# Optimization experiments

Measured on AMD Instinct MI355X. Metric: run time of the kernel, lower is better.

## Reference

```python
import jax, jax.numpy as jnp
import numpy as np

K = 20      # self.k in OurModel
TAU = 1.0   # self.tau in OurModel


def _knn_feats(emb, idx, yctx):
    # emb: [N, E] embedding table; idx: [B] int query ids; yctx: [B, N] residual context
    a = emb[idx]                                            # [B, E] gathered query embeddings
    # squared euclidean via gram trick, then sqrt == torch.cdist(p=2)
    d2 = (jnp.sum(a * a, axis=-1, keepdims=True)
          + jnp.sum(emb * emb, axis=-1)[None, :]
          - 2.0 * a @ emb.T)                                 # [B, N]
    sim = jnp.sqrt(jnp.clip(d2, 0.0, None)) + 0.001
    rows = jnp.arange(idx.shape[0])
    sim = sim.at[rows, idx].set(0.0)                         # zero self-distance
    w = jnp.exp(-sim / TAU)                                  # [B, N], self weight == 1 (max)
    # top (K+1) weights; drop the largest (the self entry) -> top-K neighbours.
    # Matches torch argsort(w)[:, -(K+1):-1]; downstream ops are order-invariant reductions.
    topw, topi = jax.lax.top_k(w, K + 1)
    topw = topw[:, 1:]                                       # [B, K]
    sel = jnp.take_along_axis(yctx, topi[:, 1:], axis=1)     # [B, K]
    f1 = jnp.sum(topw, axis=1)                               # sum of weights
    f2 = jnp.sum(sel * topw, axis=1) / jnp.sum(topw, axis=1) # weighted mean
    f3 = jnp.std(sel, axis=1, ddof=1)                        # torch.std is unbiased
    return f1, f2, f3


def _forward(emb0, emb1, rctx0, rctx1, idx0, idx1, mean_in, std_in,
             W1, b1, Wm, bm, Ws, bs):
    a1, a2, a3 = _knn_feats(emb0, idx0, rctx0)
    b1_, b2_, b3_ = _knn_feats(emb1, idx1, rctx1)
    # torch.cat(final1 + final2 + final3 + [mean, std]) column order
    feats = jnp.stack([a1, b1_, a2, b2_, a3, b3_, mean_in, std_in], axis=1)  # [B, 8]
    h = jnp.maximum(feats @ W1 + b1, 0.0)                    # [B, 64]
    mean_out = h @ Wm + bm[0]                                # [B]
    std_out = h @ Ws + bs[0]                                 # [B]
    return mean_out, std_out


def setup_inputs() -> dict:
    key = jax.random.key(0)
    ks = jax.random.split(key, 14)
    B, N, E, H = 512, 50000, 16, 64
    return {
        "emb0": jax.random.normal(ks[0], (N, E), jnp.float32),
        "emb1": jax.random.normal(ks[1], (N, E), jnp.float32),
        "rctx0": jax.random.normal(ks[2], (B, N), jnp.float32),
        "rctx1": jax.random.normal(ks[3], (B, N), jnp.float32),
        "idx0": jax.random.randint(ks[4], (B,), 0, N, jnp.int32),
        "idx1": jax.random.randint(ks[5], (B,), 0, N, jnp.int32),
        "mean_in": jax.random.normal(ks[6], (B,), jnp.float32),
        "std_in": jax.random.normal(ks[7], (B,), jnp.float32),
        "W1": jax.random.normal(ks[8], (8, H), jnp.float32) * 0.1,
        "b1": jax.random.normal(ks[9], (H,), jnp.float32) * 0.1,
        "Wm": jax.random.normal(ks[10], (H,), jnp.float32) * 0.1,
        "bm": jax.random.normal(ks[11], (1,), jnp.float32) * 0.1,
        "Ws": jax.random.normal(ks[12], (H,), jnp.float32) * 0.1,
        "bs": jax.random.normal(ks[13], (1,), jnp.float32) * 0.1,
    }


def reference(emb0, emb1, rctx0, rctx1, idx0, idx1, mean_in, std_in,
              W1, b1, Wm, bm, Ws, bs):
    return _forward(emb0, emb1, rctx0, rctx1, idx0, idx1, mean_in, std_in,
                    W1, b1, Wm, bm, Ws, bs)
```

## Files before the change

kernel.cpp:

```cpp
#include <hip/hip_runtime.h>
#include <math.h>

typedef unsigned long long u64;
#define INF64 0xFFFFFFFFFFFFFFFFULL
#define FBIG 3.3e38f
#define NTA 256
#define KSEL 20
#define QB 4
#define CNK 8
#define PREF 4
#define CAP 384

static __device__ __forceinline__ u64 umin64(u64 a, u64 b) { return a < b ? a : b; }

static __device__ __forceinline__ float dot16(
    float4 a0, float4 a1, float4 a2, float4 a3,
    float4 b0, float4 b1, float4 b2, float4 b3)
{
    float d = 0.f;
    d = fmaf(a0.x, b0.x, d); d = fmaf(a0.y, b0.y, d);
    d = fmaf(a0.z, b0.z, d); d = fmaf(a0.w, b0.w, d);
    d = fmaf(a1.x, b1.x, d); d = fmaf(a1.y, b1.y, d);
    d = fmaf(a1.z, b1.z, d); d = fmaf(a1.w, b1.w, d);
    d = fmaf(a2.x, b2.x, d); d = fmaf(a2.y, b2.y, d);
    d = fmaf(a2.z, b2.z, d); d = fmaf(a2.w, b2.w, d);
    d = fmaf(a3.x, b3.x, d); d = fmaf(a3.y, b3.y, d);
    d = fmaf(a3.z, b3.z, d); d = fmaf(a3.w, b3.w, d);
    return d;
}

__global__ __launch_bounds__(NTA) void knn_scan_kernel(
    const float* __restrict__ emb0, const float* __restrict__ emb1,
    const int* __restrict__ idx0, const int* __restrict__ idx1,
    u64* __restrict__ chunkTop, int N, int B)
{
    const int tid = threadIdx.x;
    const int lane = tid & 63;
    const int wv = tid >> 6;
    const int bx = blockIdx.x;
    const int xcd = bx & 7;
    const int s = xcd & 1;
    const int t = (bx >> 3) * 4 + (xcd >> 1);
    const int c = t & (CNK - 1);
    const int g = t >> 3;

    const float* __restrict__ emb = s ? emb1 : emb0;
    const int* __restrict__ idxp = s ? idx1 : idx0;
    const int qbase = QB * g;
    const int self0 = idxp[qbase + 0];
    const int self1 = idxp[qbase + 1];
    const int self2 = idxp[qbase + 2];
    const int self3 = idxp[qbase + 3];

    const int chunkLen = (N + CNK - 1) / CNK;
    const int jbeg = c * chunkLen;
    const int jend = min(N, jbeg + chunkLen);

    float4 q00, q01, q02, q03, q10, q11, q12, q13;
    float4 q20, q21, q22, q23, q30, q31, q32, q33;
    { const float4* p = (const float4*)(emb + (size_t)self0 * 16); q00 = p[0]; q01 = p[1]; q02 = p[2]; q03 = p[3]; }
    { const float4* p = (const float4*)(emb + (size_t)self1 * 16); q10 = p[0]; q11 = p[1]; q12 = p[2]; q13 = p[3]; }
    { const float4* p = (const float4*)(emb + (size_t)self2 * 16); q20 = p[0]; q21 = p[1]; q22 = p[2]; q23 = p[3]; }
    { const float4* p = (const float4*)(emb + (size_t)self3 * 16); q30 = p[0]; q31 = p[1]; q32 = p[2]; q33 = p[3]; }
    const float na0 = dot16(q00, q01, q02, q03, q00, q01, q02, q03);
    const float na1 = dot16(q10, q11, q12, q13, q10, q11, q12, q13);
    const float na2 = dot16(q20, q21, q22, q23, q20, q21, q22, q23);
    const float na3 = dot16(q30, q31, q32, q33, q30, q31, q32, q33);

    __shared__ float sminf[QB][NTA];
    __shared__ u64 sbuf[QB][CAP];
    __shared__ int scnt[QB];
    __shared__ float sboundf[QB];

    float mn0 = FBIG, mn1 = FBIG, mn2 = FBIG, mn3 = FBIG;
#pragma unroll
    for (int k = 0; k < PREF; ++k) {
        const int j = jbeg + (k << 8) + tid;
        const float4* p = (const float4*)(emb + (size_t)j * 16);
        float4 e0 = p[0], e1 = p[1], e2 = p[2], e3 = p[3];
        const float ne = dot16(e0, e1, e2, e3, e0, e1, e2, e3);
        float dd;
        dd = fmaxf(fmaf(dot16(q00, q01, q02, q03, e0, e1, e2, e3), -2.f, na0 + ne), 0.f); mn0 = fminf(mn0, dd);
        dd = fmaxf(fmaf(dot16(q10, q11, q12, q13, e0, e1, e2, e3), -2.f, na1 + ne), 0.f); mn1 = fminf(mn1, dd);
        dd = fmaxf(fmaf(dot16(q20, q21, q22, q23, e0, e1, e2, e3), -2.f, na2 + ne), 0.f); mn2 = fminf(mn2, dd);
        dd = fmaxf(fmaf(dot16(q30, q31, q32, q33, e0, e1, e2, e3), -2.f, na3 + ne), 0.f); mn3 = fminf(mn3, dd);
    }
    sminf[0][tid] = mn0; sminf[1][tid] = mn1; sminf[2][tid] = mn2; sminf[3][tid] = mn3;
    if (tid < QB) scnt[tid] = 0;
    __syncthreads();

    {
        float v0 = sminf[wv][lane];
        float v1 = sminf[wv][lane + 64];
        float v2 = sminf[wv][lane + 128];
        float v3 = sminf[wv][lane + 192];
        float gm = 0.f;
        for (int r = 0; r < KSEL + 1; ++r) {
            float cm = fminf(fminf(v0, v1), fminf(v2, v3));
#pragma unroll
            for (int o = 32; o; o >>= 1) cm = fminf(cm, __shfl_xor(cm, o, 64));
            gm = cm;
            if (v0 == gm) v0 = FBIG;
            if (v1 == gm) v1 = FBIG;
            if (v2 == gm) v2 = FBIG;
            if (v3 == gm) v3 = FBIG;
        }
        if (lane == 0) sboundf[wv] = __uint_as_float(__float_as_uint(gm) + 2);
    }
    __syncthreads();
    const float bnd0 = sboundf[0], bnd1 = sboundf[1];
    const float bnd2 = sboundf[2], bnd3 = sboundf[3];

    for (int j = jbeg + tid; j < jend; j += NTA) {
        const float4* p = (const float4*)(emb + (size_t)j * 16);
        float4 e0 = p[0], e1 = p[1], e2 = p[2], e3 = p[3];
        const float ne = dot16(e0, e1, e2, e3, e0, e1, e2, e3);
        const float dd0 = fmaxf(fmaf(dot16(q00, q01, q02, q03, e0, e1, e2, e3), -2.f, na0 + ne), 0.f);
        const float dd1 = fmaxf(fmaf(dot16(q10, q11, q12, q13, e0, e1, e2, e3), -2.f, na1 + ne), 0.f);
        const float dd2 = fmaxf(fmaf(dot16(q20, q21, q22, q23, e0, e1, e2, e3), -2.f, na2 + ne), 0.f);
        const float dd3 = fmaxf(fmaf(dot16(q30, q31, q32, q33, e0, e1, e2, e3), -2.f, na3 + ne), 0.f);
        if (dd0 <= bnd0 && j != self0) {
            int sl = atomicAdd(&scnt[0], 1);
            if (sl < CAP) sbuf[0][sl] = ((u64)__float_as_uint(dd0) << 32) | (unsigned)j;
        }
        if (dd1 <= bnd1 && j != self1) {
            int sl = atomicAdd(&scnt[1], 1);
            if (sl < CAP) sbuf[1][sl] = ((u64)__float_as_uint(dd1) << 32) | (unsigned)j;
        }
        if (dd2 <= bnd2 && j != self2) {
            int sl = atomicAdd(&scnt[2], 1);
            if (sl < CAP) sbuf[2][sl] = ((u64)__float_as_uint(dd2) << 32) | (unsigned)j;
        }
        if (dd3 <= bnd3 && j != self3) {
            int sl = atomicAdd(&scnt[3], 1);
            if (sl < CAP) sbuf[3][sl] = ((u64)__float_as_uint(dd3) << 32) | (unsigned)j;
        }
    }
    __syncthreads();

    {
        const int M = min(scnt[wv], CAP);
        u64 t0 = (lane < M)       ? sbuf[wv][lane]       : INF64;
        u64 t1 = (lane + 64 < M)  ? sbuf[wv][lane + 64]  : INF64;
        u64 t2 = (lane + 128 < M) ? sbuf[wv][lane + 128] : INF64;
        u64 t3 = (lane + 192 < M) ? sbuf[wv][lane + 192] : INF64;
        u64 t4 = (lane + 256 < M) ? sbuf[wv][lane + 256] : INF64;
        u64 t5 = (lane + 320 < M) ? sbuf[wv][lane + 320] : INF64;
        u64 keep = INF64;
        for (int r = 0; r < KSEL; ++r) {
            u64 cm = umin64(umin64(umin64(t0, t1), umin64(t2, t3)), umin64(t4, t5));
#pragma unroll
            for (int o = 32; o; o >>= 1) cm = umin64(cm, __shfl_xor(cm, o, 64));
            if (t0 == cm) t0 = INF64;
            if (t1 == cm) t1 = INF64;
            if (t2 == cm) t2 = INF64;
            if (t3 == cm) t3 = INF64;
            if (t4 == cm) t4 = INF64;
            if (t5 == cm) t5 = INF64;
            if (lane == r) keep = cm;
        }
        if (lane < KSEL)
            chunkTop[(((size_t)(s * B + qbase + wv)) * CNK + c) * KSEL + lane] = keep;
    }
}

__global__ __launch_bounds__(128) void merge_mlp_kernel(
    const u64* __restrict__ chunkTop,
    const float* __restrict__ rctx0, const float* __restrict__ rctx1,
    const float* __restrict__ mean_in, const float* __restrict__ std_in,
    const float* __restrict__ W1, const float* __restrict__ b1,
    const float* __restrict__ Wm, const float* __restrict__ bm,
    const float* __restrict__ Ws, const float* __restrict__ bs,
    float* __restrict__ out, int N, int B)
{
    const int b = blockIdx.x;
    const int tid = threadIdx.x;
    const int s = tid >> 6;
    const int lane = tid & 63;
    __shared__ float sf[8];

    const u64* src = chunkTop + ((size_t)(s * B + b)) * CNK * KSEL;
    u64 v0 = src[lane];
    u64 v1 = src[lane + 64];
    u64 v2 = (lane < CNK * KSEL - 128) ? src[lane + 128] : INF64;
    u64 keep = INF64;
    for (int r = 0; r < KSEL; ++r) {
        u64 cm = umin64(v0, umin64(v1, v2));
#pragma unroll
        for (int o = 32; o; o >>= 1) cm = umin64(cm, __shfl_xor(cm, o, 64));
        if (v0 == cm) v0 = INF64;
        if (v1 == cm) v1 = INF64;
        if (v2 == cm) v2 = INF64;
        if (lane == r) keep = cm;
    }
    float w = 0.f, sv = 0.f;
    if (lane < KSEL) {
        float d2 = __uint_as_float((unsigned int)(keep >> 32));
        int j = (int)(unsigned int)(keep & 0xFFFFFFFFULL);
        float sim = sqrtf(d2) + 0.001f;
        w = expf(-sim);
        const float* __restrict__ rctx = s ? rctx1 : rctx0;
        sv = rctx[(size_t)b * N + j];
    }
    float sw = w, ssw = sv * w, ss = sv, ss2 = sv * sv;
#pragma unroll
    for (int o = 32; o; o >>= 1) {
        sw  += __shfl_down(sw,  o, 64);
        ssw += __shfl_down(ssw, o, 64);
        ss  += __shfl_down(ss,  o, 64);
        ss2 += __shfl_down(ss2, o, 64);
    }
    if (lane == 0) {
        sf[0 + s] = sw;
        sf[2 + s] = ssw / sw;
        float mean = ss * (1.f / KSEL);
        float var = (ss2 - (float)KSEL * mean * mean) * (1.f / (KSEL - 1));
        sf[4 + s] = sqrtf(fmaxf(var, 0.f));
        if (s == 0) { sf[6] = mean_in[b]; sf[7] = std_in[b]; }
    }
    __syncthreads();

    if (tid < 64) {
        float f0 = sf[0], f1 = sf[1], f2 = sf[2], f3 = sf[3];
        float f4 = sf[4], f5 = sf[5], f6 = sf[6], f7 = sf[7];
        float h = b1[lane];
        h = fmaf(f0, W1[0 * 64 + lane], h);
        h = fmaf(f1, W1[1 * 64 + lane], h);
        h = fmaf(f2, W1[2 * 64 + lane], h);
        h = fmaf(f3, W1[3 * 64 + lane], h);
        h = fmaf(f4, W1[4 * 64 + lane], h);
        h = fmaf(f5, W1[5 * 64 + lane], h);
        h = fmaf(f6, W1[6 * 64 + lane], h);
        h = fmaf(f7, W1[7 * 64 + lane], h);
        h = fmaxf(h, 0.f);
        float mo = h * Wm[lane], so = h * Ws[lane];
#pragma unroll
        for (int o = 32; o; o >>= 1) {
            mo += __shfl_down(mo, o, 64);
            so += __shfl_down(so, o, 64);
        }
        if (lane == 0) {
            out[b] = mo + bm[0];
            out[B + b] = so + bs[0];
        }
    }
}

extern "C" void kernel_launch(void* const* d_in, const int* in_sizes, int n_in,
                              void* d_out, int out_size, void* d_ws, size_t ws_size,
                              hipStream_t stream) {
    const float* emb0    = (const float*)d_in[0];
    const float* emb1    = (const float*)d_in[1];
    const float* rctx0   = (const float*)d_in[2];
    const float* rctx1   = (const float*)d_in[3];
    const int*   idx0    = (const int*)d_in[4];
    const int*   idx1    = (const int*)d_in[5];
    const float* mean_in = (const float*)d_in[6];
    const float* std_in  = (const float*)d_in[7];
    const float* W1      = (const float*)d_in[8];
    const float* b1      = (const float*)d_in[9];
    const float* Wm      = (const float*)d_in[10];
    const float* bm      = (const float*)d_in[11];
    const float* Ws      = (const float*)d_in[12];
    const float* bs      = (const float*)d_in[13];

    const int B = in_sizes[4];
    const int N = in_sizes[0] / 16;

    u64* chunkTop = (u64*)d_ws;

    knn_scan_kernel<<<dim3(2 * (B / QB) * CNK), NTA, 0, stream>>>(
        emb0, emb1, idx0, idx1, chunkTop, N, B);

    merge_mlp_kernel<<<dim3(B), 128, 0, stream>>>(
        chunkTop, rctx0, rctx1, mean_in, std_in,
        W1, b1, Wm, bm, Ws, bs, (float*)d_out, N, B);
}
```

Measured before the change: 301.7 us.

## Compute KNN distances with split-bf16 MFMA tiles and exact candidate rescoring

Replaces the per-thread scalar FP32 distance loop with 32x32x16 bf16 MFMA tiles. Each embedding is split into hi/lo bf16 parts so three MFMAs approximate the fp32 dot product. A separate kernel precomputes the embedding norms, and each block now handles 32 queries and 16 chunks, so embedding reuse across queries goes up. Candidates within a slack (DEPS=0.5) of the approximate threshold are rescored exactly in fp32 before top-k selection. The risks are approximation error versus the slack margin and overflow of the smaller candidate capacity, which is now 256.

```diff
diff --git a/kernel.cpp b/kernel.cpp
--- a/kernel.cpp
+++ b/kernel.cpp
@@ -2,16 +2,33 @@
 #include <math.h>
 
 typedef unsigned long long u64;
+typedef unsigned int u32;
 #define INF64 0xFFFFFFFFFFFFFFFFULL
 #define FBIG 3.3e38f
-#define NTA 256
 #define KSEL 20
-#define QB 4
-#define CNK 8
-#define PREF 4
-#define CAP 384
+#define QT   32
+#define CNK  16
+#define CAP  256
+#define PREFT 4
+#define DEPS 0.5f
+#define NTHR 512
+
+typedef __bf16 bf16x8 __attribute__((ext_vector_type(8)));
+typedef float  f32x16 __attribute__((ext_vector_type(16)));
+typedef unsigned int uint4e __attribute__((ext_vector_type(4)));
 
 static __device__ __forceinline__ u64 umin64(u64 a, u64 b) { return a < b ? a : b; }
+static __device__ __forceinline__ u32 asu(float f) { return __builtin_bit_cast(u32, f); }
+static __device__ __forceinline__ float trunchi(u32 u) { return __builtin_bit_cast(float, u & 0xffff0000u); }
+#define PERM2(a,b) __builtin_amdgcn_perm((a),(b),0x07060302u)
+static __device__ __forceinline__ bf16x8 mk8(u32 a, u32 b, u32 c, u32 d) {
+    uint4e t = {a, b, c, d};
+    return __builtin_bit_cast(bf16x8, t);
+}
+static __device__ __forceinline__ f32x16 zero16() {
+    f32x16 z = {0.f,0.f,0.f,0.f,0.f,0.f,0.f,0.f,0.f,0.f,0.f,0.f,0.f,0.f,0.f,0.f};
+    return z;
+}
 
 static __device__ __forceinline__ float dot16(
     float4 a0, float4 a1, float4 a2, float4 a3,
@@ -29,138 +46,212 @@
     return d;
 }
 
-__global__ __launch_bounds__(NTA) void knn_scan_kernel(
+static __device__ __forceinline__ void cvt_hilo(float4 f0, float4 f1, bf16x8& hi, bf16x8& lo) {
+    u32 u0=asu(f0.x),u1=asu(f0.y),u2=asu(f0.z),u3=asu(f0.w);
+    u32 u4=asu(f1.x),u5=asu(f1.y),u6=asu(f1.z),u7=asu(f1.w);
+    hi = mk8(PERM2(u1,u0), PERM2(u3,u2), PERM2(u5,u4), PERM2(u7,u6));
+    u32 w0=asu(f0.x-trunchi(u0)), w1=asu(f0.y-trunchi(u1));
+    u32 w2=asu(f0.z-trunchi(u2)), w3=asu(f0.w-trunchi(u3));
+    u32 w4=asu(f1.x-trunchi(u4)), w5=asu(f1.y-trunchi(u5));
+    u32 w6=asu(f1.z-trunchi(u6)), w7=asu(f1.w-trunchi(u7));
+    lo = mk8(PERM2(w1,w0), PERM2(w3,w2), PERM2(w5,w4), PERM2(w7,w6));
+}
+
+static __device__ __forceinline__ f32x16 tile_qe(
+    const float* __restrict__ embS, int base, int col, int kb, int N,
+    bf16x8 B1, bf16x8 B2)
+{
+    int row = base + col;
+    row = min(row, N - 1);
+    const float4* ep = (const float4*)(embS + (size_t)row * 16 + kb * 8);
+    float4 f0 = ep[0], f1 = ep[1];
+    bf16x8 A1, A2;
+    cvt_hilo(f0, f1, A1, A2);
+    f32x16 acc = zero16();
+    acc = __builtin_amdgcn_mfma_f32_32x32x16_bf16(A1, B1, acc, 0, 0, 0);
+    acc = __builtin_amdgcn_mfma_f32_32x32x16_bf16(A1, B2, acc, 0, 0, 0);
+    acc = __builtin_amdgcn_mfma_f32_32x32x16_bf16(A2, B1, acc, 0, 0, 0);
+    return acc;
+}
+
+__global__ __launch_bounds__(256) void norm_kernel(
+    const float* __restrict__ emb0, const float* __restrict__ emb1,
+    float* __restrict__ neBuf, int N, int npad)
+{
+    const int j = blockIdx.x * 256 + threadIdx.x;
+    const float* __restrict__ e = blockIdx.y ? emb1 : emb0;
+    float* __restrict__ o = neBuf + (size_t)blockIdx.y * npad;
+    float v = FBIG;
+    if (j < N) {
+        const float4* p = (const float4*)(e + (size_t)j * 16);
+        float4 e0=p[0],e1=p[1],e2=p[2],e3=p[3];
+        v = dot16(e0,e1,e2,e3, e0,e1,e2,e3);
+    }
+    if (j < npad) o[j] = v;
+}
+
+__global__ __launch_bounds__(NTHR, 4) void knn_scan_kernel(
     const float* __restrict__ emb0, const float* __restrict__ emb1,
     const int* __restrict__ idx0, const int* __restrict__ idx1,
-    u64* __restrict__ chunkTop, int N, int B)
-{
-    const int tid = threadIdx.x;
+    const float* __restrict__ neBuf,
+    u64* __restrict__ chunkTop, int N, int B, int chlen)
+{
+    const int tid  = threadIdx.x;
     const int lane = tid & 63;
-    const int wv = tid >> 6;
-    const int bx = blockIdx.x;
-    const int xcd = bx & 7;
-    const int s = xcd & 1;
-    const int t = (bx >> 3) * 4 + (xcd >> 1);
-    const int c = t & (CNK - 1);
-    const int g = t >> 3;
-
-    const float* __restrict__ emb = s ? emb1 : emb0;
-    const int* __restrict__ idxp = s ? idx1 : idx0;
-    const int qbase = QB * g;
-    const int self0 = idxp[qbase + 0];
-    const int self1 = idxp[qbase + 1];
-    const int self2 = idxp[qbase + 2];
-    const int self3 = idxp[qbase + 3];
-
-    const int chunkLen = (N + CNK - 1) / CNK;
-    const int jbeg = c * chunkLen;
-    const int jend = min(N, jbeg + chunkLen);
-
-    float4 q00, q01, q02, q03, q10, q11, q12, q13;
-    float4 q20, q21, q22, q23, q30, q31, q32, q33;
-    { const float4* p = (const float4*)(emb + (size_t)self0 * 16); q00 = p[0]; q01 = p[1]; q02 = p[2]; q03 = p[3]; }
-    { const float4* p = (const float4*)(emb + (size_t)self1 * 16); q10 = p[0]; q11 = p[1]; q12 = p[2]; q13 = p[3]; }
-    { const float4* p = (const float4*)(emb + (size_t)self2 * 16); q20 = p[0]; q21 = p[1]; q22 = p[2]; q23 = p[3]; }
-    { const float4* p = (const float4*)(emb + (size_t)self3 * 16); q30 = p[0]; q31 = p[1]; q32 = p[2]; q33 = p[3]; }
-    const float na0 = dot16(q00, q01, q02, q03, q00, q01, q02, q03);
-    const float na1 = dot16(q10, q11, q12, q13, q10, q11, q12, q13);
-    const float na2 = dot16(q20, q21, q22, q23, q20, q21, q22, q23);
-    const float na3 = dot16(q30, q31, q32, q33, q30, q31, q32, q33);
-
-    __shared__ float sminf[QB][NTA];
-    __shared__ u64 sbuf[QB][CAP];
-    __shared__ int scnt[QB];
-    __shared__ float sboundf[QB];
-
-    float mn0 = FBIG, mn1 = FBIG, mn2 = FBIG, mn3 = FBIG;
-#pragma unroll
-    for (int k = 0; k < PREF; ++k) {
-        const int j = jbeg + (k << 8) + tid;
-        const float4* p = (const float4*)(emb + (size_t)j * 16);
-        float4 e0 = p[0], e1 = p[1], e2 = p[2], e3 = p[3];
-        const float ne = dot16(e0, e1, e2, e3, e0, e1, e2, e3);
-        float dd;
-        dd = fmaxf(fmaf(dot16(q00, q01, q02, q03, e0, e1, e2, e3), -2.f, na0 + ne), 0.f); mn0 = fminf(mn0, dd);
-        dd = fmaxf(fmaf(dot16(q10, q11, q12, q13, e0, e1, e2, e3), -2.f, na1 + ne), 0.f); mn1 = fminf(mn1, dd);
-        dd = fmaxf(fmaf(dot16(q20, q21, q22, q23, e0, e1, e2, e3), -2.f, na2 + ne), 0.f); mn2 = fminf(mn2, dd);
-        dd = fmaxf(fmaf(dot16(q30, q31, q32, q33, e0, e1, e2, e3), -2.f, na3 + ne), 0.f); mn3 = fminf(mn3, dd);
-    }
-    sminf[0][tid] = mn0; sminf[1][tid] = mn1; sminf[2][tid] = mn2; sminf[3][tid] = mn3;
-    if (tid < QB) scnt[tid] = 0;
-    __syncthreads();
-
+    const int wv   = tid >> 6;
+    const int col  = lane & 31;
+    const int kb   = lane >> 5;
+    const int bx   = blockIdx.x;
+    const int xcd  = bx & 7;
+    const int s    = xcd & 1;
+    const int t_   = (bx >> 3) * 4 + (xcd >> 1);
+    const int c    = t_ & (CNK - 1);
+    const int qt   = t_ >> 4;
+    const int qbase = qt * QT;
+    const int jbeg = c * chlen;
+    const int tpc  = chlen >> 5;
+    const int npad = chlen * CNK;
+
+    const float* __restrict__ embS = s ? emb1 : emb0;
+    const int*   __restrict__ idxp = s ? idx1 : idx0;
+    const float* __restrict__ neS  = neBuf + (size_t)s * npad;
+
+    __shared__ float Qs[QT][16];
+    __shared__ float naS[QT];
+    __shared__ int   sq[QT];
+    __shared__ int   scnt[QT];
+    __shared__ float sthr[QT];
+    __shared__ float sMin[QT][32];
+    __shared__ u32   sbuf[QT][CAP];
+
+    if (tid < QT) { sq[tid] = idxp[qbase + tid]; scnt[tid] = 0; }
+    __syncthreads();
+    if (tid < 128) {
+        int q = tid >> 2, part = tid & 3;
+        ((float4*)(&Qs[q][0]))[part] = ((const float4*)(embS + (size_t)sq[q] * 16))[part];
+    }
+    __syncthreads();
+    if (tid < QT) {
+        const float4* qp = (const float4*)(&Qs[tid][0]);
+        float4 a0=qp[0],a1=qp[1],a2=qp[2],a3=qp[3];
+        naS[tid] = dot16(a0,a1,a2,a3, a0,a1,a2,a3);
+    }
+    bf16x8 B1, B2;
     {
-        float v0 = sminf[wv][lane];
-        float v1 = sminf[wv][lane + 64];
-        float v2 = sminf[wv][lane + 128];
-        float v3 = sminf[wv][lane + 192];
+        const float4* qp = (const float4*)(&Qs[col][kb * 8]);
+        float4 f0 = qp[0], f1 = qp[1];
+        cvt_hilo(f0, f1, B1, B2);
+    }
+    __syncthreads();
+
+    const float na_l  = naS[col];
+    const int   self_l = sq[col];
+
+    float m0v = FBIG, m1v = FBIG;
+#define PINS(r, nef) { float v_ = fmaf(acc[r], -2.f, na_l + (nef)); \
+    float t1_ = fminf(m1v, fmaxf(m0v, v_)); m0v = fminf(m0v, v_); m1v = t1_; }
+    for (int pt = 0; pt < PREFT; ++pt) {
+        const int t = wv + pt * 8;
+        const int base = jbeg + t * 32;
+        const float4* np_ = (const float4*)(neS + base + kb * 4);
+        float4 n0 = np_[0], n1 = np_[2], n2 = np_[4], n3 = np_[6];
+        f32x16 acc = tile_qe(embS, base, col, kb, N, B1, B2);
+        PINS(0,n0.x)  PINS(1,n0.y)  PINS(2,n0.z)  PINS(3,n0.w)
+        PINS(4,n1.x)  PINS(5,n1.y)  PINS(6,n1.z)  PINS(7,n1.w)
+        PINS(8,n2.x)  PINS(9,n2.y)  PINS(10,n2.z) PINS(11,n2.w)
+        PINS(12,n3.x) PINS(13,n3.y) PINS(14,n3.z) PINS(15,n3.w)
+    }
+#undef PINS
+    sMin[col][(wv * 2 + kb) * 2 + 0] = m0v;
+    sMin[col][(wv * 2 + kb) * 2 + 1] = m1v;
+    __syncthreads();
+
+    for (int qq = 0; qq < 4; ++qq) {
+        const int q = wv * 4 + qq;
+        float v = (lane < 32) ? sMin[q][lane] : FBIG;
         float gm = 0.f;
         for (int r = 0; r < KSEL + 1; ++r) {
-            float cm = fminf(fminf(v0, v1), fminf(v2, v3));
+            float cm = v;
 #pragma unroll
             for (int o = 32; o; o >>= 1) cm = fminf(cm, __shfl_xor(cm, o, 64));
             gm = cm;
-            if (v0 == gm) v0 = FBIG;
-            if (v1 == gm) v1 = FBIG;
-            if (v2 == gm) v2 = FBIG;
-            if (v3 == gm) v3 = FBIG;
-        }
-        if (lane == 0) sboundf[wv] = __uint_as_float(__float_as_uint(gm) + 2);
-    }
-    __syncthreads();
-    const float bnd0 = sboundf[0], bnd1 = sboundf[1];
-    const float bnd2 = sboundf[2], bnd3 = sboundf[3];
-
-    for (int j = jbeg + tid; j < jend; j += NTA) {
-        const float4* p = (const float4*)(emb + (size_t)j * 16);
-        float4 e0 = p[0], e1 = p[1], e2 = p[2], e3 = p[3];
-        const float ne = dot16(e0, e1, e2, e3, e0, e1, e2, e3);
-        const float dd0 = fmaxf(fmaf(dot16(q00, q01, q02, q03, e0, e1, e2, e3), -2.f, na0 + ne), 0.f);
-        const float dd1 = fmaxf(fmaf(dot16(q10, q11, q12, q13, e0, e1, e2, e3), -2.f, na1 + ne), 0.f);
-        const float dd2 = fmaxf(fmaf(dot16(q20, q21, q22, q23, e0, e1, e2, e3), -2.f, na2 + ne), 0.f);
-        const float dd3 = fmaxf(fmaf(dot16(q30, q31, q32, q33, e0, e1, e2, e3), -2.f, na3 + ne), 0.f);
-        if (dd0 <= bnd0 && j != self0) {
-            int sl = atomicAdd(&scnt[0], 1);
-            if (sl < CAP) sbuf[0][sl] = ((u64)__float_as_uint(dd0) << 32) | (unsigned)j;
-        }
-        if (dd1 <= bnd1 && j != self1) {
-            int sl = atomicAdd(&scnt[1], 1);
-            if (sl < CAP) sbuf[1][sl] = ((u64)__float_as_uint(dd1) << 32) | (unsigned)j;
-        }
-        if (dd2 <= bnd2 && j != self2) {
-            int sl = atomicAdd(&scnt[2], 1);
-            if (sl < CAP) sbuf[2][sl] = ((u64)__float_as_uint(dd2) << 32) | (unsigned)j;
-        }
-        if (dd3 <= bnd3 && j != self3) {
-            int sl = atomicAdd(&scnt[3], 1);
-            if (sl < CAP) sbuf[3][sl] = ((u64)__float_as_uint(dd3) << 32) | (unsigned)j;
-        }
-    }
-    __syncthreads();
-
-    {
-        const int M = min(scnt[wv], CAP);
-        u64 t0 = (lane < M)       ? sbuf[wv][lane]       : INF64;
-        u64 t1 = (lane + 64 < M)  ? sbuf[wv][lane + 64]  : INF64;
-        u64 t2 = (lane + 128 < M) ? sbuf[wv][lane + 128] : INF64;
-        u64 t3 = (lane + 192 < M) ? sbuf[wv][lane + 192] : INF64;
-        u64 t4 = (lane + 256 < M) ? sbuf[wv][lane + 256] : INF64;
-        u64 t5 = (lane + 320 < M) ? sbuf[wv][lane + 320] : INF64;
+            if (v == gm) v = FBIG;
+        }
+        if (lane == 0) sthr[q] = gm + DEPS;
+    }
+    __syncthreads();
+    const float thr_l = sthr[col];
+
+#define EPI(r, nef) { float ad_ = fmaf(acc[r], -2.f, na_l + (nef)); \
+    if (ad_ <= thr_l) msk |= (1u << (r)); }
+    for (int t = wv; t < tpc; t += 8) {
+        const int base = jbeg + t * 32;
+        const float4* np_ = (const float4*)(neS + base + kb * 4);
+        float4 n0 = np_[0], n1 = np_[2], n2 = np_[4], n3 = np_[6];
+        f32x16 acc = tile_qe(embS, base, col, kb, N, B1, B2);
+        u32 msk = 0;
+        EPI(0,n0.x)  EPI(1,n0.y)  EPI(2,n0.z)  EPI(3,n0.w)
+        EPI(4,n1.x)  EPI(5,n1.y)  EPI(6,n1.z)  EPI(7,n1.w)
+        EPI(8,n2.x)  EPI(9,n2.y)  EPI(10,n2.z) EPI(11,n2.w)
+        EPI(12,n3.x) EPI(13,n3.y) EPI(14,n3.z) EPI(15,n3.w)
+        if (msk) {
+#pragma unroll
+            for (int r = 0; r < 16; ++r) if (msk & (1u << r)) {
+                int j = base + (r & 3) + 8 * (r >> 2) + 4 * kb;
+                if (j != self_l) {
+                    int sl = atomicAdd(&scnt[col], 1);
+                    if (sl < CAP) sbuf[col][sl] = (u32)j;
+                }
+            }
+        }
+    }
+#undef EPI
+    __syncthreads();
+
+    for (int qq = 0; qq < 4; ++qq) {
+        const int q = wv * 4 + qq;
+        const int M = min(scnt[q], CAP);
+        const float4* qp = (const float4*)(&Qs[q][0]);
+        const float4 q0=qp[0], q1=qp[1], q2=qp[2], q3=qp[3];
+        const float naq = naS[q];
+        auto rk = [&](int i) -> u64 {
+            int j = (int)sbuf[q][i];
+            const float4* p = (const float4*)(embS + (size_t)j * 16);
+            float4 e0=p[0],e1=p[1],e2=p[2],e3=p[3];
+            float ne_ = dot16(e0,e1,e2,e3, e0,e1,e2,e3);
+            float qe  = dot16(q0,q1,q2,q3, e0,e1,e2,e3);
+            float dd  = fmaxf(fmaf(qe, -2.f, naq + ne_), 0.f);
+            return ((u64)asu(dd) << 32) | (u32)j;
+        };
+        u64 k0 = INF64, k1 = INF64, k2 = INF64, k3 = INF64;
+        if (lane < M)       k0 = rk(lane);
+        if (lane + 64 < M)  k1 = rk(lane + 64);
+        if (lane + 128 < M) k2 = rk(lane + 128);
+        if (lane + 192 < M) k3 = rk(lane + 192);
         u64 keep = INF64;
-        for (int r = 0; r < KSEL; ++r) {
-            u64 cm = umin64(umin64(umin64(t0, t1), umin64(t2, t3)), umin64(t4, t5));
-#pragma unroll
-            for (int o = 32; o; o >>= 1) cm = umin64(cm, __shfl_xor(cm, o, 64));
-            if (t0 == cm) t0 = INF64;
-            if (t1 == cm) t1 = INF64;
-            if (t2 == cm) t2 = INF64;
-            if (t3 == cm) t3 = INF64;
-            if (t4 == cm) t4 = INF64;
-            if (t5 == cm) t5 = INF64;
-            if (lane == r) keep = cm;
+        if (M <= 128) {
+            for (int r = 0; r < KSEL; ++r) {
+                u64 cm = umin64(k0, k1);
+#pragma unroll
+                for (int o = 32; o; o >>= 1) cm = umin64(cm, __shfl_xor(cm, o, 64));
+                if (k0 == cm) k0 = INF64;
+                if (k1 == cm) k1 = INF64;
+                if (lane == r) keep = cm;
+            }
+        } else {
+            for (int r = 0; r < KSEL; ++r) {
+                u64 cm = umin64(umin64(k0, k1), umin64(k2, k3));
+#pragma unroll
+                for (int o = 32; o; o >>= 1) cm = umin64(cm, __shfl_xor(cm, o, 64));
+                if (k0 == cm) k0 = INF64;
+                if (k1 == cm) k1 = INF64;
+                if (k2 == cm) k2 = INF64;
+                if (k3 == cm) k3 = INF64;
+                if (lane == r) keep = cm;
+            }
         }
         if (lane < KSEL)
-            chunkTop[(((size_t)(s * B + qbase + wv)) * CNK + c) * KSEL + lane] = keep;
+            chunkTop[((size_t)(s * B + qbase + q) * CNK + c) * KSEL + lane] = keep;
     }
 }
 
@@ -179,18 +270,22 @@
     const int lane = tid & 63;
     __shared__ float sf[8];
 
-    const u64* src = chunkTop + ((size_t)(s * B + b)) * CNK * KSEL;
+    const u64* src = chunkTop + ((size_t)(s * B + b)) * (CNK * KSEL);
     u64 v0 = src[lane];
     u64 v1 = src[lane + 64];
-    u64 v2 = (lane < CNK * KSEL - 128) ? src[lane + 128] : INF64;
+    u64 v2 = src[lane + 128];
+    u64 v3 = src[lane + 192];
+    u64 v4 = src[lane + 256];
     u64 keep = INF64;
     for (int r = 0; r < KSEL; ++r) {
-        u64 cm = umin64(v0, umin64(v1, v2));
+        u64 cm = umin64(umin64(umin64(v0, v1), umin64(v2, v3)), v4);
 #pragma unroll
         for (int o = 32; o; o >>= 1) cm = umin64(cm, __shfl_xor(cm, o, 64));
         if (v0 == cm) v0 = INF64;
         if (v1 == cm) v1 = INF64;
         if (v2 == cm) v2 = INF64;
+        if (v3 == cm) v3 = INF64;
+        if (v4 == cm) v4 = INF64;
         if (lane == r) keep = cm;
     }
     float w = 0.f, sv = 0.f;
@@ -267,10 +362,16 @@
     const int B = in_sizes[4];
     const int N = in_sizes[0] / 16;
 
-    u64* chunkTop = (u64*)d_ws;
-
-    knn_scan_kernel<<<dim3(2 * (B / QB) * CNK), NTA, 0, stream>>>(
-        emb0, emb1, idx0, idx1, chunkTop, N, B);
+    int chlen = (((N + CNK - 1) / CNK) + 31) & ~31;
+    int npad  = chlen * CNK;
+
+    float* neBuf = (float*)d_ws;
+    u64* chunkTop = (u64*)((char*)d_ws + (size_t)2 * npad * sizeof(float));
+
+    norm_kernel<<<dim3(npad / 256, 2), 256, 0, stream>>>(emb0, emb1, neBuf, N, npad);
+
+    knn_scan_kernel<<<dim3(2 * (B / QT) * CNK), NTHR, 0, stream>>>(
+        emb0, emb1, idx0, idx1, neBuf, chunkTop, N, B, chlen);
 
     merge_mlp_kernel<<<dim3(B), 128, 0, stream>>>(
         chunkTop, rctx0, rctx1, mean_in, std_in,
```

Measured after the change: 311.0 us. 1.03x slower.
